# Kernel tuning notes

Hardware: AMD Instinct MI355X
Metric: run time of the kernel (lower is better)

Reference implementation:

```python
import math
import jax, jax.numpy as jnp
import numpy as np

K_EACH = 64
EPS = 1e-5
EPS_VAR = 1e-4
_GELU_C = math.sqrt(2.0 / math.pi)


def _gelu(x):
    return 0.5 * x * (1.0 + jnp.tanh(_GELU_C * (x + 0.044715 * x * x * x)))


def _topk_mask(score, k):
    # score: [B,T,D] -> bool mask [B,T,D] with True at the top-k per row
    B, T, D = score.shape
    idx = jax.lax.top_k(score, k)[1].reshape(B * T, k)
    rows = jnp.arange(B * T)[:, None]
    m = jnp.zeros((B * T, D), dtype=bool).at[rows, idx].set(True)
    return m.reshape(B, T, D)


def setup_inputs() -> dict:
    key = jax.random.key(0)
    ks = jax.random.split(key, 6)
    B, T, D = 4, 4096, 2048
    x = jax.random.normal(ks[0], (B, T, D), dtype=jnp.float32)
    ema_mean = 0.1 * jax.random.normal(ks[1], (D,), dtype=jnp.float32)
    ema_sq = ema_mean ** 2 + jax.random.uniform(ks[2], (D,), dtype=jnp.float32, minval=0.5, maxval=1.5)
    ema_out_mean = 0.1 * jax.random.normal(ks[3], (D,), dtype=jnp.float32)
    ema_out_sq = ema_out_mean ** 2 + jax.random.uniform(ks[4], (D,), dtype=jnp.float32, minval=0.5, maxval=1.5)
    d_raw = jax.random.normal(ks[5], (D,), dtype=jnp.float32)
    ema_out_dir = d_raw / jnp.linalg.norm(d_raw)
    return {
        "x": x,
        "logit_decay": jnp.asarray(math.log(0.9 / 0.1), jnp.float32),
        "log_tau": jnp.asarray(math.log(2.0), jnp.float32),
        "log_beta": jnp.asarray(math.log(math.exp(0.5) - 1.0), jnp.float32),
        "log_gamma": jnp.asarray(math.log(math.exp(1.0) - 1.0), jnp.float32),
        "ema_mean": ema_mean,
        "ema_sq": ema_sq,
        "ema_out_mean": ema_out_mean,
        "ema_out_sq": ema_out_sq,
        "ema_out_dir": ema_out_dir,
    }


def reference(x, logit_decay, log_tau, log_beta, log_gamma,
              ema_mean, ema_sq, ema_out_mean, ema_out_sq, ema_out_dir):
    # Steady-state (_ready=True) forward of GELU205. logit_decay only affects
    # the EMA state update (a no-grad side effect), not the returned output.
    sg = jax.lax.stop_gradient
    D = x.shape[-1]
    k = min(K_EACH, D)

    tau = jnp.exp(log_tau)
    beta = jax.nn.softplus(log_beta)
    gamma = jax.nn.softplus(log_gamma)

    out = _gelu(x)

    # per-channel z-scores against running stats (no-grad in original)
    var_in = jnp.maximum(ema_sq - ema_mean ** 2, EPS_VAR)
    z_in = sg((sg(x) - ema_mean) / (jnp.sqrt(var_in) + EPS))
    var_out = jnp.maximum(ema_out_sq - ema_out_mean ** 2, EPS_VAR)
    z_out = sg((sg(out) - ema_out_mean) / (jnp.sqrt(var_out) + EPS))

    # dual top-k intersection mask
    mask_in = _topk_mask(jnp.abs(z_in), k)
    mask_out = _topk_mask(jnp.abs(z_out), k)
    inter = mask_in & mask_out

    # channel gate (grads flow to beta, gamma; z_in is detached)
    inter_g = jnp.clip(1.0 + beta * jnp.tanh(gamma * z_in), 0.1, 8.0)
    gate_vec = jnp.where(inter, inter_g, 1.0)

    # cosine-similarity gate (fully no-grad in original, incl. tau)
    out_n = out / jnp.maximum(jnp.linalg.norm(out, axis=-1, keepdims=True), 1e-12)
    ema_n = ema_out_dir / jnp.maximum(jnp.linalg.norm(ema_out_dir), 1e-12)
    cos_sim = jnp.clip(jnp.sum(out_n * ema_n, axis=-1), -1.0, 1.0)
    gate_cos = sg(jnp.exp(-tau * cos_sim))[..., None]

    return out * gate_vec * gate_cos
```

## Files before the change

kernel.cpp:

```cpp
#include <hip/hip_runtime.h>
#include <math.h>
#include <stdint.h>

#define D_    2048
#define BLK   256
#define KSEL  64
#define NBIN  1024
#define CAP   128

typedef float v2f __attribute__((ext_vector_type(2)));

__device__ __forceinline__ float tanh_xla(float x) {
    const float kMax = 7.90531110763549805f;
    float xc = fminf(fmaxf(x, -kMax), kMax);
    float x2 = __fmul_rn(xc, xc);
    float p = -2.76076847742355e-16f;
    p = __fadd_rn(__fmul_rn(p, x2), 2.00018790482477e-13f);
    p = __fadd_rn(__fmul_rn(p, x2), -8.60467152213735e-11f);
    p = __fadd_rn(__fmul_rn(p, x2), 5.12229709037114e-08f);
    p = __fadd_rn(__fmul_rn(p, x2), 1.48572235717979e-05f);
    p = __fadd_rn(__fmul_rn(p, x2), 6.37261928875436e-04f);
    p = __fadd_rn(__fmul_rn(p, x2), 4.89352455891786e-03f);
    float num = __fmul_rn(xc, p);
    float q = 1.19825839466702e-06f;
    q = __fadd_rn(__fmul_rn(q, x2), 1.18534705686654e-04f);
    q = __fadd_rn(__fmul_rn(q, x2), 2.26843463243900e-03f);
    q = __fadd_rn(__fmul_rn(q, x2), 4.89352518554385e-03f);
    float r = __fdiv_rn(num, q);
    return (fabsf(x) < 0.0004f) ? x : r;
}

__device__ __forceinline__ float gelu_exact(float xx) {
    float a = __fmul_rn(0.044715f, xx);
    a = __fmul_rn(a, xx);
    a = __fmul_rn(a, xx);
    float inner = __fadd_rn(xx, a);
    float tg = tanh_xla(__fmul_rn(0.7978845608028654f, inner));
    return __fmul_rn(__fmul_rn(0.5f, xx), __fadd_rn(1.0f, tg));
}

__device__ __forceinline__ float tanh_fast(float y) {
    float e = __expf(2.0f * y);
    return 1.0f - 2.0f * __builtin_amdgcn_rcpf(1.0f + e);
}

__global__ __launch_bounds__(BLK) void prep_kernel(
    const float* __restrict__ m_in, const float* __restrict__ q_in,
    const float* __restrict__ m_out, const float* __restrict__ q_out,
    const float* __restrict__ dirv,
    const float* __restrict__ p_log_tau,
    const float* __restrict__ p_log_beta,
    const float* __restrict__ p_log_gamma,
    float* __restrict__ wsp)
{
    __shared__ float spart[4];
    const int t = threadIdx.x;
    const int c = blockIdx.x * BLK + t;
    if (c < D_) {
        float mi = m_in[c];
        float vi = fmaxf(__fsub_rn(q_in[c], __fmul_rn(mi, mi)), 1e-4f);
        float di = __fadd_rn(__fsqrt_rn(vi), 1e-5f);
        wsp[c]        = di;
        wsp[D_ + c]   = __fdiv_rn(1.0f, di);
        float mo = m_out[c];
        float vo = fmaxf(__fsub_rn(q_out[c], __fmul_rn(mo, mo)), 1e-4f);
        float dd = __fadd_rn(__fsqrt_rn(vo), 1e-5f);
        wsp[2 * D_ + c] = dd;
        wsp[3 * D_ + c] = __fdiv_rn(1.0f, dd);
    }
    if (blockIdx.x == 0) {
        float acc = 0.f;
        #pragma unroll
        for (int k = 0; k < D_ / BLK; ++k) {
            float v = dirv[t + k * BLK];
            acc = fmaf(v, v, acc);
        }
        #pragma unroll
        for (int off = 32; off > 0; off >>= 1) acc += __shfl_xor(acc, off);
        if ((t & 63) == 0) spart[t >> 6] = acc;
        __syncthreads();
        if (t == 0) {
            wsp[4 * D_ + 0] = spart[0] + spart[1] + spart[2] + spart[3];
            wsp[4 * D_ + 1] = expf(p_log_tau[0]);
            wsp[4 * D_ + 2] = log1pf(expf(p_log_beta[0]));
            wsp[4 * D_ + 3] = log1pf(expf(p_log_gamma[0]));
        }
    }
}

__global__ __launch_bounds__(BLK) void gelu205_kernel(
    const float* __restrict__ x,
    const float* __restrict__ ema_mean,
    const float* __restrict__ ema_out_mean,
    const float* __restrict__ ema_out_dir,
    const float* __restrict__ wsp,
    float* __restrict__ out)
{
    __shared__ uint32_t hist[2 * NBIN];
    __shared__ uint32_t cbI[CAP], ciI[CAP], cfI[CAP];
    __shared__ uint32_t cbO[CAP], ciO[CAP], cfO[CAP];
    __shared__ float sred[8];
    __shared__ float sgcos;
    __shared__ int sBi, sGi, sNCi, sBo, sGo, sNCo;

    const int t = threadIdx.x;
    const int row = blockIdx.x;
    const float* xr = x + (size_t)row * D_;
    float* outr = out + (size_t)row * D_;

    const float* den_in  = wsp;
    const float* inv_in  = wsp + D_;
    const float* den_out = wsp + 2 * D_;
    const float* inv_out = wsp + 3 * D_;
    const float dd_row = wsp[4 * D_ + 0];
    const float tau    = wsp[4 * D_ + 1];
    const float beta   = wsp[4 * D_ + 2];
    const float gamma  = wsp[4 * D_ + 3];

    float ov[8], zif[8];
    int bin_in[8], bin_out[8];
    v2f acc_oo = {0.f, 0.f}, acc_od = {0.f, 0.f};

    #pragma unroll
    for (int g = 0; g < 2; ++g) {
        const int base = (g << 10) + t * 4;
        float4 x4  = *(const float4*)(xr + base);
        float4 m4  = *(const float4*)(ema_mean + base);
        float4 i4  = *(const float4*)(inv_in + base);
        float4 mo4 = *(const float4*)(ema_out_mean + base);
        float4 io4 = *(const float4*)(inv_out + base);
        float4 d4  = *(const float4*)(ema_out_dir + base);
        const v2f* xp2  = (const v2f*)&x4;
        const v2f* mp2  = (const v2f*)&m4;
        const v2f* ip2  = (const v2f*)&i4;
        const v2f* mop2 = (const v2f*)&mo4;
        const v2f* iop2 = (const v2f*)&io4;
        const v2f* dp2  = (const v2f*)&d4;
        #pragma unroll
        for (int p = 0; p < 2; ++p) {
            const int j = g * 4 + p * 2;
            v2f xx = xp2[p];
            v2f x2 = xx * xx;
            v2f ax = xx * 0.044715f;
            v2f inner = __builtin_elementwise_fma(ax, x2, xx);
            v2f ea = inner * -1.5957691216057308f;
            v2f ev; ev.x = __expf(ea.x); ev.y = __expf(ea.y);
            v2f dn = ev + 1.0f;
            v2f sgm; sgm.x = __builtin_amdgcn_rcpf(dn.x);
            sgm.y = __builtin_amdgcn_rcpf(dn.y);
            v2f o2 = xx * sgm;
            ov[j] = o2.x; ov[j + 1] = o2.y;
            v2f zi2 = (xx - mp2[p]) * ip2[p];
            zif[j] = zi2.x; zif[j + 1] = zi2.y;
            bin_in[j]     = (int)fminf(fabsf(zi2.x) * 128.0f, 1023.0f);
            bin_in[j + 1] = (int)fminf(fabsf(zi2.y) * 128.0f, 1023.0f);
            v2f zo2 = (o2 - mop2[p]) * iop2[p];
            bin_out[j]     = (int)fminf(fabsf(zo2.x) * 128.0f, 1023.0f);
            bin_out[j + 1] = (int)fminf(fabsf(zo2.y) * 128.0f, 1023.0f);
            acc_oo = __builtin_elementwise_fma(o2, o2, acc_oo);
            acc_od = __builtin_elementwise_fma(o2, dp2[p], acc_od);
        }
    }
    float s_oo = acc_oo.x + acc_oo.y;
    float s_od = acc_od.x + acc_od.y;

    #pragma unroll
    for (int off = 32; off > 0; off >>= 1) {
        s_oo += __shfl_xor(s_oo, off);
        s_od += __shfl_xor(s_od, off);
    }
    const int wid = t >> 6, lane = t & 63;
    if (lane == 0) {
        sred[wid * 2 + 0] = s_oo;
        sred[wid * 2 + 1] = s_od;
    }

    {
        uint4 z4 = make_uint4(0u, 0u, 0u, 0u);
        *(uint4*)&hist[t * 8]     = z4;
        *(uint4*)&hist[t * 8 + 4] = z4;
    }
    if (t == 0) { sNCi = 0; sNCo = 0; }
    __syncthreads();

    #pragma unroll
    for (int j = 0; j < 8; ++j) {
        atomicAdd(&hist[bin_in[j]], 1u);
        atomicAdd(&hist[NBIN + bin_out[j]], 1u);
    }
    if (t == 0) {
        float oo = sred[0] + sred[2] + sred[4] + sred[6];
        float od = sred[1] + sred[3] + sred[5] + sred[7];
        float no = fmaxf(sqrtf(oo), 1e-12f);
        float nd = fmaxf(sqrtf(dd_row), 1e-12f);
        float cs = fminf(fmaxf(od / (no * nd), -1.0f), 1.0f);
        sgcos = expf(-tau * cs);
    }
    __syncthreads();

    if (wid < 2) {
        const uint32_t* hp = hist + wid * NBIN;
        uint32_t h[16];
        *(uint4*)&h[0]  = *(const uint4*)&hp[lane * 16 + 0];
        *(uint4*)&h[4]  = *(const uint4*)&hp[lane * 16 + 4];
        *(uint4*)&h[8]  = *(const uint4*)&hp[lane * 16 + 8];
        *(uint4*)&h[12] = *(const uint4*)&hp[lane * 16 + 12];
        uint32_t tot = 0;
        #pragma unroll
        for (int k = 0; k < 16; ++k) tot += h[k];
        uint32_t S = tot;
        #pragma unroll
        for (int d2 = 1; d2 < 64; d2 <<= 1) {
            uint32_t o = __shfl_down(S, d2, 64);
            S += (lane + d2 < 64) ? o : 0u;
        }
        uint32_t run = S - tot;
        #pragma unroll
        for (int k = 15; k >= 0; --k) {
            uint32_t prev = run;
            run += h[k];
            if (run >= (uint32_t)KSEL && prev < (uint32_t)KSEL) {
                if (wid == 0) { sBi = lane * 16 + k; sGi = (int)prev; }
                else          { sBo = lane * 16 + k; sGo = (int)prev; }
            }
        }
    }
    __syncthreads();

    const int Bi = sBi, Bo = sBo;
    int slotI[8], slotO[8];

    #pragma unroll
    for (int j = 0; j < 8; ++j) {
        slotI[j] = -1;
        slotO[j] = -1;
        const int ch = ((j >> 2) << 10) + t * 4 + (j & 3);
        if (bin_in[j] == Bi) {
            float xx = xr[ch];
            float ze = fabsf(__fdiv_rn(__fsub_rn(xx, ema_mean[ch]), den_in[ch]));
            int sl = atomicAdd(&sNCi, 1);
            if (sl < CAP) {
                cbI[sl] = __float_as_uint(ze);
                ciI[sl] = (uint32_t)ch;
                slotI[j] = sl;
            }
        }
        if (bin_out[j] == Bo) {
            float xx = xr[ch];
            float oe = gelu_exact(xx);
            float ze = fabsf(__fdiv_rn(__fsub_rn(oe, ema_out_mean[ch]), den_out[ch]));
            int sl = atomicAdd(&sNCo, 1);
            if (sl < CAP) {
                cbO[sl] = __float_as_uint(ze);
                ciO[sl] = (uint32_t)ch;
                slotO[j] = sl;
            }
        }
    }
    __syncthreads();

    {
        const int nci = min(sNCi, CAP), nco = min(sNCo, CAP);
        const uint32_t needI = (uint32_t)(KSEL - sGi);
        const uint32_t needO = (uint32_t)(KSEL - sGo);
        if (t < 128) {
            for (int i = t; i < nci; i += 128) {
                uint32_t ui = cbI[i], di = ciI[i], r = 0;
                for (int jj = 0; jj < nci; ++jj) {
                    uint32_t uj = cbI[jj];
                    r += (uj > ui || (uj == ui && ciI[jj] < di)) ? 1u : 0u;
                }
                cfI[i] = (r < needI) ? 1u : 0u;
            }
        } else {
            for (int i = t - 128; i < nco; i += 128) {
                uint32_t ui = cbO[i], di = ciO[i], r = 0;
                for (int jj = 0; jj < nco; ++jj) {
                    uint32_t uj = cbO[jj];
                    r += (uj > ui || (uj == ui && ciO[jj] < di)) ? 1u : 0u;
                }
                cfO[i] = (r < needO) ? 1u : 0u;
            }
        }
    }
    __syncthreads();

    const float gcos = sgcos;
    #pragma unroll
    for (int g = 0; g < 2; ++g) {
        float4 r4;
        float* rp = (float*)&r4;
        #pragma unroll
        for (int l = 0; l < 4; ++l) {
            const int j = g * 4 + l;
            bool selI = (bin_in[j] > Bi) || (slotI[j] >= 0 && cfI[slotI[j]] != 0u);
            bool selO = (bin_out[j] > Bo) || (slotO[j] >= 0 && cfO[slotO[j]] != 0u);
            float gate = 1.0f;
            if (selI && selO) {
                float th = tanh_fast(gamma * zif[j]);
                gate = fminf(fmaxf(fmaf(beta, th, 1.0f), 0.1f), 8.0f);
            }
            rp[l] = ov[j] * gate * gcos;
        }
        *(float4*)(outr + (g << 10) + t * 4) = r4;
    }
}

extern "C" void kernel_launch(void* const* d_in, const int* in_sizes, int n_in,
                              void* d_out, int out_size, void* d_ws, size_t ws_size,
                              hipStream_t stream) {
    const float* x            = (const float*)d_in[0];
    const float* p_log_tau    = (const float*)d_in[2];
    const float* p_log_beta   = (const float*)d_in[3];
    const float* p_log_gamma  = (const float*)d_in[4];
    const float* ema_mean     = (const float*)d_in[5];
    const float* ema_sq       = (const float*)d_in[6];
    const float* ema_out_mean = (const float*)d_in[7];
    const float* ema_out_sq   = (const float*)d_in[8];
    const float* ema_out_dir  = (const float*)d_in[9];
    float* wsp = (float*)d_ws;
    const int rows = in_sizes[0] / D_;

    prep_kernel<<<(D_ + BLK - 1) / BLK, BLK, 0, stream>>>(
        ema_mean, ema_sq, ema_out_mean, ema_out_sq, ema_out_dir,
        p_log_tau, p_log_beta, p_log_gamma, wsp);
    gelu205_kernel<<<rows, BLK, 0, stream>>>(
        x, ema_mean, ema_out_mean, ema_out_dir, wsp,
        (float*)d_out);
}
```

Measured before the change: 76.02 us.

## Halve histogram bins, skip low-z atomics with fallback, use exp2 intrinsics

Result: no change. 75.03 us, median of 2 (-1.3%).

```diff
diff --git a/kernel.cpp b/kernel.cpp
--- a/kernel.cpp
+++ b/kernel.cpp
@@ -5,7 +5,8 @@
 #define D_    2048
 #define BLK   256
 #define KSEL  64
-#define NBIN  1024
+#define NBIN  512
+#define B0    96
 #define CAP   128
 
 typedef float v2f __attribute__((ext_vector_type(2)));
@@ -40,7 +41,7 @@
 }
 
 __device__ __forceinline__ float tanh_fast(float y) {
-    float e = __expf(2.0f * y);
+    float e = __builtin_amdgcn_exp2f(y * 2.8853900817779268f);
     return 1.0f - 2.0f * __builtin_amdgcn_rcpf(1.0f + e);
 }
 
@@ -88,6 +89,37 @@
     }
 }
 
+__device__ __forceinline__ void scan_find(
+    const uint32_t* hist, int wid, int lane,
+    int* sBi, int* sGi, int* sBo, int* sGo)
+{
+    if (wid < 2) {
+        const uint32_t* hp = hist + wid * NBIN;
+        uint32_t h[8];
+        *(uint4*)&h[0] = *(const uint4*)&hp[lane * 8 + 0];
+        *(uint4*)&h[4] = *(const uint4*)&hp[lane * 8 + 4];
+        uint32_t tot = 0;
+        #pragma unroll
+        for (int k = 0; k < 8; ++k) tot += h[k];
+        uint32_t S = tot;
+        #pragma unroll
+        for (int d2 = 1; d2 < 64; d2 <<= 1) {
+            uint32_t o = __shfl_down(S, d2, 64);
+            S += (lane + d2 < 64) ? o : 0u;
+        }
+        uint32_t run = S - tot;
+        #pragma unroll
+        for (int k = 7; k >= 0; --k) {
+            uint32_t prev = run;
+            run += h[k];
+            if (run >= (uint32_t)KSEL && prev < (uint32_t)KSEL) {
+                if (wid == 0) { *sBi = lane * 8 + k; *sGi = (int)prev; }
+                else          { *sBo = lane * 8 + k; *sGo = (int)prev; }
+            }
+        }
+    }
+}
+
 __global__ __launch_bounds__(BLK) void gelu205_kernel(
     const float* __restrict__ x,
     const float* __restrict__ ema_mean,
@@ -143,8 +175,9 @@
             v2f x2 = xx * xx;
             v2f ax = xx * 0.044715f;
             v2f inner = __builtin_elementwise_fma(ax, x2, xx);
-            v2f ea = inner * -1.5957691216057308f;
-            v2f ev; ev.x = __expf(ea.x); ev.y = __expf(ea.y);
+            v2f ea = inner * -2.3022269136469443f;
+            v2f ev; ev.x = __builtin_amdgcn_exp2f(ea.x);
+            ev.y = __builtin_amdgcn_exp2f(ea.y);
             v2f dn = ev + 1.0f;
             v2f sgm; sgm.x = __builtin_amdgcn_rcpf(dn.x);
             sgm.y = __builtin_amdgcn_rcpf(dn.y);
@@ -152,11 +185,11 @@
             ov[j] = o2.x; ov[j + 1] = o2.y;
             v2f zi2 = (xx - mp2[p]) * ip2[p];
             zif[j] = zi2.x; zif[j + 1] = zi2.y;
-            bin_in[j]     = (int)fminf(fabsf(zi2.x) * 128.0f, 1023.0f);
-            bin_in[j + 1] = (int)fminf(fabsf(zi2.y) * 128.0f, 1023.0f);
+            bin_in[j]     = (int)fminf(fabsf(zi2.x) * 64.0f, 511.0f);
+            bin_in[j + 1] = (int)fminf(fabsf(zi2.y) * 64.0f, 511.0f);
             v2f zo2 = (o2 - mop2[p]) * iop2[p];
-            bin_out[j]     = (int)fminf(fabsf(zo2.x) * 128.0f, 1023.0f);
-            bin_out[j + 1] = (int)fminf(fabsf(zo2.y) * 128.0f, 1023.0f);
+            bin_out[j]     = (int)fminf(fabsf(zo2.x) * 64.0f, 511.0f);
+            bin_out[j + 1] = (int)fminf(fabsf(zo2.y) * 64.0f, 511.0f);
             acc_oo = __builtin_elementwise_fma(o2, o2, acc_oo);
             acc_od = __builtin_elementwise_fma(o2, dp2[p], acc_od);
         }
@@ -175,18 +208,14 @@
         sred[wid * 2 + 1] = s_od;
     }
 
-    {
-        uint4 z4 = make_uint4(0u, 0u, 0u, 0u);
-        *(uint4*)&hist[t * 8]     = z4;
-        *(uint4*)&hist[t * 8 + 4] = z4;
-    }
-    if (t == 0) { sNCi = 0; sNCo = 0; }
+    *(uint4*)&hist[t * 4] = make_uint4(0u, 0u, 0u, 0u);
+    if (t == 0) { sNCi = 0; sNCo = 0; sBi = -1; sBo = -1; }
     __syncthreads();
 
     #pragma unroll
     for (int j = 0; j < 8; ++j) {
-        atomicAdd(&hist[bin_in[j]], 1u);
-        atomicAdd(&hist[NBIN + bin_out[j]], 1u);
+        if (bin_in[j] >= B0)  atomicAdd(&hist[bin_in[j]], 1u);
+        if (bin_out[j] >= B0) atomicAdd(&hist[NBIN + bin_out[j]], 1u);
     }
     if (t == 0) {
         float oo = sred[0] + sred[2] + sred[4] + sred[6];
@@ -198,38 +227,23 @@
     }
     __syncthreads();
 
-    if (wid < 2) {
-        const uint32_t* hp = hist + wid * NBIN;
-        uint32_t h[16];
-        *(uint4*)&h[0]  = *(const uint4*)&hp[lane * 16 + 0];
-        *(uint4*)&h[4]  = *(const uint4*)&hp[lane * 16 + 4];
-        *(uint4*)&h[8]  = *(const uint4*)&hp[lane * 16 + 8];
-        *(uint4*)&h[12] = *(const uint4*)&hp[lane * 16 + 12];
-        uint32_t tot = 0;
-        #pragma unroll
-        for (int k = 0; k < 16; ++k) tot += h[k];
-        uint32_t S = tot;
-        #pragma unroll
-        for (int d2 = 1; d2 < 64; d2 <<= 1) {
-            uint32_t o = __shfl_down(S, d2, 64);
-            S += (lane + d2 < 64) ? o : 0u;
-        }
-        uint32_t run = S - tot;
-        #pragma unroll
-        for (int k = 15; k >= 0; --k) {
-            uint32_t prev = run;
-            run += h[k];
-            if (run >= (uint32_t)KSEL && prev < (uint32_t)KSEL) {
-                if (wid == 0) { sBi = lane * 16 + k; sGi = (int)prev; }
-                else          { sBo = lane * 16 + k; sGo = (int)prev; }
-            }
-        }
-    }
-    __syncthreads();
-
-    const int Bi = sBi, Bo = sBo;
+    scan_find(hist, wid, lane, &sBi, &sGi, &sBo, &sGo);
+    __syncthreads();
+
+    int Bi = sBi, Bo = sBo;
+    if (Bi < 0 || Bo < 0) {
+        #pragma unroll
+        for (int j = 0; j < 8; ++j) {
+            if (bin_in[j] < B0)  atomicAdd(&hist[bin_in[j]], 1u);
+            if (bin_out[j] < B0) atomicAdd(&hist[NBIN + bin_out[j]], 1u);
+        }
+        __syncthreads();
+        scan_find(hist, wid, lane, &sBi, &sGi, &sBo, &sGo);
+        __syncthreads();
+        Bi = sBi; Bo = sBo;
+    }
+
     int slotI[8], slotO[8];
-
     #pragma unroll
     for (int j = 0; j < 8; ++j) {
         slotI[j] = -1;
```
